# Kernel optimization log

Hardware: AMD Instinct MI355X
Metric: run time of the kernel (lower is better)

## Reference

```python
import jax, jax.numpy as jnp
import numpy as np

B, P, N = 1024, 100, 101
EMB, H, DK = 128, 8, 16
SQRT_EMB = 11.313708498984761
CLIP = 10.0


def setup_inputs() -> dict:
    key = jax.random.key(0)
    ks = jax.random.split(key, 12)
    inp = {
        "encoded_last_node": jax.random.normal(ks[0], (B, P, EMB), jnp.float32),
        "load": jax.random.uniform(ks[1], (B, P), jnp.float32),
        "time": jax.random.uniform(ks[2], (B, P), jnp.float32),
        "length": jax.random.uniform(ks[3], (B, P), jnp.float32),
        "route_open": jax.random.uniform(ks[4], (B, P), jnp.float32),
        "ninf_mask": jnp.zeros((B, P, N), jnp.float32),
        "encoded_nodes": jax.random.normal(ks[5], (B, N, EMB), jnp.float32),
        # weights stored [in, out]
        "Wq": jax.random.normal(ks[6], (EMB + 4, H * DK), jnp.float32) * 0.05,
        "Wk": jax.random.normal(ks[7], (EMB, H * DK), jnp.float32) * 0.05,
        "Wv": jax.random.normal(ks[8], (EMB, H * DK), jnp.float32) * 0.05,
        "Wc": jax.random.normal(ks[9], (H * DK, EMB), jnp.float32) * 0.05,
        "bc": jax.random.normal(ks[10], (EMB,), jnp.float32) * 0.05,
    }
    return inp


def _heads(x):
    # [B, n, H*DK] -> [B, H, n, DK]
    b, n, _ = x.shape
    return x.reshape(b, n, H, DK).transpose(0, 2, 1, 3)


def reference(encoded_last_node, load, time, length, route_open, ninf_mask,
              encoded_nodes, Wq, Wk, Wv, Wc, bc):
    # set_kv
    k = _heads(encoded_nodes @ Wk)            # [B,H,N,DK]
    v = _heads(encoded_nodes @ Wv)            # [B,H,N,DK]
    # forward
    input_cat = jnp.concatenate(
        [encoded_last_node, load[:, :, None], time[:, :, None],
         length[:, :, None], route_open[:, :, None]], axis=2)  # [B,P,EMB+4]
    q = _heads(input_cat @ Wq)                # [B,H,P,DK]
    score = jnp.einsum('bhpd,bhnd->bhpn', q, k) / jnp.sqrt(jnp.float32(DK))
    score = score + ninf_mask[:, None, :, :]
    weights = jax.nn.softmax(score, axis=3)
    out = jnp.einsum('bhpn,bhnd->bhpd', weights, v)
    out_concat = out.transpose(0, 2, 1, 3).reshape(out.shape[0], out.shape[2], H * DK)
    mh = out_concat @ Wc + bc                 # [B,P,EMB]
    score2 = jnp.einsum('bpe,bne->bpn', mh, encoded_nodes) / SQRT_EMB
    score2 = CLIP * jnp.tanh(score2) + ninf_mask
    probs = jax.nn.softmax(score2, axis=2)
    return probs
```

## Files before the change

### kernel.cpp

```cpp
#include <hip/hip_runtime.h>
#include <stdint.h>

#define B_    1024
#define P_    100
#define N_    101
#define EMB_  128
#define H_    8
#define DK_   16

#define ROWS  112
#define KSTR  136

typedef uint16_t bf16;
typedef __attribute__((ext_vector_type(8))) short short8;
typedef __attribute__((ext_vector_type(4))) float float4v;

struct F4 { float x, y, z, w; };

#define L2E 1.4426950408889634f

#if __has_builtin(__builtin_amdgcn_exp2f)
#define EXP2(x) __builtin_amdgcn_exp2f(x)
#else
#define EXP2(x) exp2f(x)
#endif
#if __has_builtin(__builtin_amdgcn_rcpf)
#define RCP(x) __builtin_amdgcn_rcpf(x)
#else
#define RCP(x) (1.0f / (x))
#endif

__device__ __forceinline__ float b2f(bf16 u) {
    union { uint32_t i; float f; } c; c.i = ((uint32_t)u) << 16; return c.f;
}
__device__ __forceinline__ bf16 f2b(float f) {
    union { float f; uint32_t i; } c; c.f = f;
    return (bf16)((c.i + 0x8000u) >> 16);
}
__device__ __forceinline__ uint32_t pk2(float a, float b) {
    union { float f; uint32_t i; } ca, cb; ca.f = a; cb.f = b;
    return __builtin_amdgcn_perm(cb.i + 0x8000u, ca.i + 0x8000u, 0x07060302u);
}

__device__ __forceinline__ void stage_m(const float* __restrict__ src, int nrows,
                                        bf16* __restrict__ dst, int tid) {
    for (int i = tid; i < ROWS * 32; i += 1024) {
        int r = i >> 5, c = (i & 31) << 2;
        uint32_t p0 = 0, p1 = 0;
        if (r < nrows) {
            float4 v = *(const float4*)(src + (size_t)r * EMB_ + c);
            p0 = pk2(v.x, v.y); p1 = pk2(v.z, v.w);
        }
        uint32_t* d = (uint32_t*)(dst + r * KSTR + c);
        d[0] = p0; d[1] = p1;
    }
}

__global__ __launch_bounds__(256)
void prep_wT(const float* __restrict__ Wq, const float* __restrict__ Wk,
             const float* __restrict__ Wv, const float* __restrict__ Wc,
             bf16* __restrict__ ws) {
    int idx = blockIdx.x * 256 + threadIdx.x;
    int w = idx >> 14, rem = idx & 16383;
    int k = rem >> 7, o = rem & 127;
    const float* W = (w == 0) ? Wk : (w == 1) ? Wv : (w == 2) ? Wq : Wc;
    ws[((size_t)w << 14) + o * 128 + k] = f2b(W[(size_t)k * 128 + o]);
}

__global__ __launch_bounds__(1024, 4)
void vrp_kernel(const float* __restrict__ eln,
                const float* __restrict__ load_,
                const float* __restrict__ time_,
                const float* __restrict__ len_,
                const float* __restrict__ open_,
                const float* __restrict__ mask_,
                const float* __restrict__ enc_,
                const float* __restrict__ Wq,
                const float* __restrict__ bc,
                const bf16* __restrict__ wsWT,
                float* __restrict__ out)
{
    const int b    = blockIdx.x;
    const int tid  = threadIdx.x;
    const int wave = tid >> 6;
    const int lane = tid & 63;
    const int lr = lane & 15, lq = lane >> 4, lk = lq << 3;

    __shared__ bf16 smem[78336];
    __shared__ float sS4[ROWS * 4];
    __shared__ float sWq4[4 * EMB_];
    bf16* const R1 = smem;
    bf16* const R2 = smem + 15232;
    bf16* const R3 = smem + 30464;
    bf16* const R4 = smem + 47872;
    bf16* const R5 = smem + 63104;

    const bf16* WkT = wsWT;
    const bf16* WvT = wsWT + 16384;
    const bf16* WqT = wsWT + 32768;
    const bf16* WcT = wsWT + 49152;

    const float* encB  = enc_  + (size_t)b * N_ * EMB_;
    const float* elnB  = eln   + (size_t)b * P_ * EMB_;
    const float* maskB = mask_ + (size_t)b * P_ * N_;
    float*       outB  = out   + (size_t)b * P_ * N_;

    stage_m(encB, N_, R1, tid);
    stage_m(elnB, P_, R5, tid);
    if (tid < 512) {
        int d = tid >> 2, c = 112 + ((tid & 3) << 2);
        uint32_t* z = (uint32_t*)(R3 + d * KSTR + c);
        z[0] = 0; z[1] = 0;
    }
    if (tid < ROWS * 4) {
        int r = tid >> 2, j = tid & 3;
        float v = 0.f;
        if (r < P_) {
            const float* s4 = (j == 0) ? load_ : (j == 1) ? time_
                             : (j == 2) ? len_ : open_;
            v = s4[(size_t)b * P_ + r];
        }
        sS4[r * 4 + j] = v;
    }
    if (tid < 512) {
        int j = tid >> 7, c = tid & 127;
        sWq4[j * EMB_ + c] = Wq[(size_t)(EMB_ + j) * EMB_ + c];
    }
    __syncthreads();

    {
        const int col = 16 * (wave & 7) + lr;
        const int mt0 = (wave >> 3) ? 4 : 0;
        const int mt1 = (wave >> 3) ? 7 : 4;
        short8 bk[4], bv[4], bq[4];
        {
            const bf16* rk = WkT + (size_t)col * 128 + lk;
            const bf16* rv = WvT + (size_t)col * 128 + lk;
            const bf16* rq = WqT + (size_t)col * 128 + lk;
            #pragma unroll
            for (int s = 0; s < 4; ++s) {
                bk[s] = *(const short8*)(rk + s * 32);
                bv[s] = *(const short8*)(rv + s * 32);
                bq[s] = *(const short8*)(rq + s * 32);
            }
        }
        float w0 = sWq4[col], w1 = sWq4[EMB_ + col];
        float w2 = sWq4[2 * EMB_ + col], w3 = sWq4[3 * EMB_ + col];
        for (int mt = mt0; mt < mt1; ++mt) {
            short8 a[4];
            #pragma unroll
            for (int s = 0; s < 4; ++s)
                a[s] = *(const short8*)(R1 + (mt * 16 + lr) * KSTR + s * 32 + lk);
            float4v ck = {0.f, 0.f, 0.f, 0.f}, cv = {0.f, 0.f, 0.f, 0.f};
            #pragma unroll
            for (int s = 0; s < 4; ++s) {
                ck = __builtin_amdgcn_mfma_f32_16x16x32_bf16(a[s], bk[s], ck, 0, 0, 0);
                cv = __builtin_amdgcn_mfma_f32_16x16x32_bf16(a[s], bv[s], cv, 0, 0, 0);
            }
            int n0 = mt * 16 + (lq << 2);
            #pragma unroll
            for (int r = 0; r < 4; ++r)
                R2[(n0 + r) * KSTR + col] = f2b(ck[r]);
            uint32_t* d = (uint32_t*)(R3 + col * KSTR + n0);
            d[0] = pk2(cv[0], cv[1]);
            d[1] = pk2(cv[2], cv[3]);
            short8 aq[4];
            #pragma unroll
            for (int s = 0; s < 4; ++s)
                aq[s] = *(const short8*)(R5 + (mt * 16 + lr) * KSTR + s * 32 + lk);
            float4v cq = {0.f, 0.f, 0.f, 0.f};
            #pragma unroll
            for (int s = 0; s < 4; ++s)
                cq = __builtin_amdgcn_mfma_f32_16x16x32_bf16(aq[s], bq[s], cq, 0, 0, 0);
            int row0 = mt * 16 + (lq << 2);
            #pragma unroll
            for (int r = 0; r < 4; ++r) {
                const float* s4 = sS4 + (row0 + r) * 4;
                float acc = cq[r] + s4[0] * w0 + s4[1] * w1 + s4[2] * w2 + s4[3] * w3;
                R4[(row0 + r) * KSTR + col] = f2b(acc * (0.25f * L2E));
            }
        }
    }
    __syncthreads();

    const int hg = (wave >= 7) ? 1 : 0;
    const int pt = wave - hg * 7;
    float msk2[7][4];
    float4v o4[4];
    short8 q0, q1;
    if (wave < 14) {
        {
            const int p = pt * 16 + lr;
            const bool pvalid = (p < P_);
            const float* mrow = maskB + (size_t)(pvalid ? p : 0) * N_;
            #pragma unroll
            for (int nt = 0; nt < 6; ++nt) {
                int nb = nt * 16 + (lq << 2);
                F4 mv = *(const F4*)(mrow + nb);
                msk2[nt][0] = pvalid ? mv.x * L2E : 0.f;
                msk2[nt][1] = pvalid ? mv.y * L2E : 0.f;
                msk2[nt][2] = pvalid ? mv.z * L2E : 0.f;
                msk2[nt][3] = pvalid ? mv.w * L2E : 0.f;
            }
            if (lq == 0) {
                F4 mv = *(const F4*)(mrow + 96);
                msk2[6][0] = pvalid ? mv.x * L2E : 0.f;
                msk2[6][1] = pvalid ? mv.y * L2E : 0.f;
                msk2[6][2] = pvalid ? mv.z * L2E : 0.f;
                msk2[6][3] = pvalid ? mv.w * L2E : 0.f;
            } else if (lq == 1) {
                msk2[6][0] = pvalid ? mrow[100] * L2E : 0.f;
                msk2[6][1] = -3.0e38f; msk2[6][2] = -3.0e38f; msk2[6][3] = -3.0e38f;
            } else {
                msk2[6][0] = -3.0e38f; msk2[6][1] = -3.0e38f;
                msk2[6][2] = -3.0e38f; msk2[6][3] = -3.0e38f;
            }
        }
        q0 = *(const short8*)(R4 + (pt * 16 + lr) * KSTR + hg * 64 + lk);
        q1 = *(const short8*)(R4 + (pt * 16 + lr) * KSTR + hg * 64 + 32 + lk);
    }
    __syncthreads();
    if (wave < 14) {
        bf16* Pbuf = hg ? R4 : R5;
        {
            uint32_t* z = (uint32_t*)(Pbuf + (pt * 16 + lr) * KSTR + 112 + (lq << 2));
            z[0] = 0; z[1] = 0;
        }
        #pragma unroll
        for (int hh = 0; hh < 4; ++hh) {
            int h  = hg * 4 + hh;
            int k0 = hg * 64 + (hh >> 1) * 32;
            short8 bq = (hh < 2) ? q0 : q1;
            if ((lq >> 1) != (hh & 1)) bq = (short8){0,0,0,0,0,0,0,0};
            float sc[7][4];
            #pragma unroll
            for (int nt = 0; nt < 7; ++nt) {
                short8 ak = *(const short8*)(R2 + (nt * 16 + lr) * KSTR + k0 + lk);
                float4v cc = {msk2[nt][0], msk2[nt][1], msk2[nt][2], msk2[nt][3]};
                cc = __builtin_amdgcn_mfma_f32_16x16x32_bf16(ak, bq, cc, 0, 0, 0);
                #pragma unroll
                for (int r = 0; r < 4; ++r) sc[nt][r] = cc[r];
            }
            float mm[7];
            #pragma unroll
            for (int nt = 0; nt < 7; ++nt)
                mm[nt] = fmaxf(fmaxf(sc[nt][0], sc[nt][1]),
                               fmaxf(sc[nt][2], sc[nt][3]));
            float m = fmaxf(fmaxf(fmaxf(mm[0], mm[1]), fmaxf(mm[2], mm[3])),
                            fmaxf(fmaxf(mm[4], mm[5]), mm[6]));
            m = fmaxf(m, __shfl_xor(m, 16));
            m = fmaxf(m, __shfl_xor(m, 32));
            float s0 = 0.f, s1 = 0.f, s2 = 0.f, s3 = 0.f;
            #pragma unroll
            for (int nt = 0; nt < 7; ++nt) {
                float e0 = EXP2(sc[nt][0] - m); sc[nt][0] = e0; s0 += e0;
                float e1 = EXP2(sc[nt][1] - m); sc[nt][1] = e1; s1 += e1;
                float e2 = EXP2(sc[nt][2] - m); sc[nt][2] = e2; s2 += e2;
                float e3 = EXP2(sc[nt][3] - m); sc[nt][3] = e3; s3 += e3;
            }
            float su = (s0 + s1) + (s2 + s3);
            su += __shfl_xor(su, 16);
            su += __shfl_xor(su, 32);
            float inv = RCP(su);
            #pragma unroll
            for (int nt = 0; nt < 7; ++nt) {
                uint32_t* d = (uint32_t*)(Pbuf + (pt * 16 + lr) * KSTR
                                          + nt * 16 + (lq << 2));
                d[0] = pk2(sc[nt][0] * inv, sc[nt][1] * inv);
                d[1] = pk2(sc[nt][2] * inv, sc[nt][3] * inv);
            }
            float4v o = {0.f, 0.f, 0.f, 0.f};
            #pragma unroll
            for (int ks = 0; ks < 128; ks += 32) {
                short8 a2 = *(const short8*)(Pbuf + (pt * 16 + lr) * KSTR + ks + lk);
                short8 b2 = *(const short8*)(R3 + (h * 16 + lr) * KSTR + ks + lk);
                o = __builtin_amdgcn_mfma_f32_16x16x32_bf16(a2, b2, o, 0, 0, 0);
            }
            o4[hh] = o;
        }
    }
    __syncthreads();

    if (wave < 14) {
        #pragma unroll
        for (int hh = 0; hh < 4; ++hh) {
            int h = hg * 4 + hh;
            #pragma unroll
            for (int r = 0; r < 4; ++r)
                R4[(pt * 16 + (lq << 2) + r) * KSTR + h * 16 + lr] = f2b(o4[hh][r]);
        }
    }
    __syncthreads();

    {
        const int col = 16 * (wave & 7) + lr;
        const int mt0 = (wave >> 3) ? 4 : 0;
        const int mt1 = (wave >> 3) ? 7 : 4;
        short8 bw[4];
        {
            const bf16* rc = WcT + (size_t)col * 128 + lk;
            #pragma unroll
            for (int s = 0; s < 4; ++s) bw[s] = *(const short8*)(rc + s * 32);
        }
        float bcv = bc[col];
        for (int mt = mt0; mt < mt1; ++mt) {
            short8 a[4];
            #pragma unroll
            for (int s = 0; s < 4; ++s)
                a[s] = *(const short8*)(R4 + (mt * 16 + lr) * KSTR + s * 32 + lk);
            float4v c = {0.f, 0.f, 0.f, 0.f};
            #pragma unroll
            for (int s = 0; s < 4; ++s)
                c = __builtin_amdgcn_mfma_f32_16x16x32_bf16(a[s], bw[s], c, 0, 0, 0);
            int row0 = mt * 16 + (lq << 2);
            #pragma unroll
            for (int r = 0; r < 4; ++r) {
                float m = c[r] + bcv;
                bf16 hb = f2b(m);
                R5[(row0 + r) * KSTR + col] = hb;
                R2[(row0 + r) * KSTR + col] = f2b(m - b2f(hb));
            }
        }
    }
    __syncthreads();

    if (wave < 7) {
        const int pt2 = wave;
        short8 bhi[4], blo[4];
        #pragma unroll
        for (int s = 0; s < 4; ++s) {
            bhi[s] = *(const short8*)(R5 + (pt2 * 16 + lr) * KSTR + s * 32 + lk);
            blo[s] = *(const short8*)(R2 + (pt2 * 16 + lr) * KSTR + s * 32 + lk);
        }
        float sc[7][4];
        #pragma unroll
        for (int nt = 0; nt < 7; ++nt) {
            float4v cc = {0.f, 0.f, 0.f, 0.f};
            #pragma unroll
            for (int s = 0; s < 4; ++s) {
                short8 ae = *(const short8*)(R1 + (nt * 16 + lr) * KSTR + s * 32 + lk);
                cc = __builtin_amdgcn_mfma_f32_16x16x32_bf16(ae, bhi[s], cc, 0, 0, 0);
                cc = __builtin_amdgcn_mfma_f32_16x16x32_bf16(ae, blo[s], cc, 0, 0, 0);
            }
            #pragma unroll
            for (int r = 0; r < 4; ++r) {
                float y = EXP2(cc[r] * (0.08838834764831845f * 2.0f * L2E));
                float t = fmaf(-2.0f, RCP(y + 1.0f), 1.0f);
                sc[nt][r] = fmaf(10.0f * L2E, t, msk2[nt][r]);
            }
        }
        const float mF = 10.0f * L2E;
        float s0 = 0.f, s1 = 0.f, s2 = 0.f, s3 = 0.f;
        #pragma unroll
        for (int nt = 0; nt < 7; ++nt) {
            float e0 = EXP2(sc[nt][0] - mF); sc[nt][0] = e0; s0 += e0;
            float e1 = EXP2(sc[nt][1] - mF); sc[nt][1] = e1; s1 += e1;
            float e2 = EXP2(sc[nt][2] - mF); sc[nt][2] = e2; s2 += e2;
            float e3 = EXP2(sc[nt][3] - mF); sc[nt][3] = e3; s3 += e3;
        }
        float su = (s0 + s1) + (s2 + s3);
        su += __shfl_xor(su, 16);
        su += __shfl_xor(su, 32);
        float inv = RCP(su);
        const int p = pt2 * 16 + lr;
        if (p < P_) {
            float* orow = outB + (size_t)p * N_;
            #pragma unroll
            for (int nt = 0; nt < 6; ++nt) {
                F4 ov = { sc[nt][0] * inv, sc[nt][1] * inv,
                          sc[nt][2] * inv, sc[nt][3] * inv };
                *(F4*)(orow + nt * 16 + (lq << 2)) = ov;
            }
            if (lq == 0) {
                F4 ov = { sc[6][0] * inv, sc[6][1] * inv,
                          sc[6][2] * inv, sc[6][3] * inv };
                *(F4*)(orow + 96) = ov;
            } else if (lq == 1) {
                orow[100] = sc[6][0] * inv;
            }
        }
    }
}

extern "C" void kernel_launch(void* const* d_in, const int* in_sizes, int n_in,
                              void* d_out, int out_size, void* d_ws, size_t ws_size,
                              hipStream_t stream) {
    const float* eln   = (const float*)d_in[0];
    const float* load_ = (const float*)d_in[1];
    const float* time_ = (const float*)d_in[2];
    const float* len_  = (const float*)d_in[3];
    const float* open_ = (const float*)d_in[4];
    const float* mask_ = (const float*)d_in[5];
    const float* enc_  = (const float*)d_in[6];
    const float* Wq    = (const float*)d_in[7];
    const float* Wk    = (const float*)d_in[8];
    const float* Wv    = (const float*)d_in[9];
    const float* Wc    = (const float*)d_in[10];
    const float* bc    = (const float*)d_in[11];
    float* out = (float*)d_out;
    bf16* wsWT = (bf16*)d_ws;

    prep_wT<<<dim3(256), dim3(256), 0, stream>>>(Wq, Wk, Wv, Wc, wsWT);
    vrp_kernel<<<dim3(B_), dim3(1024), 0, stream>>>(
        eln, load_, time_, len_, open_, mask_, enc_, Wq, bc, wsWT, out);
}
```

Before: 271.4 us.

## Make blocks persistent over four batches and prefetch next batch into registers

The grid shrinks from one block per batch to 256 persistent blocks that each loop over four batch elements. The next batch's encoded_nodes, last-node embeddings and scalar features are loaded into registers mid-iteration, so their global latency can overlap the attention and output compute of the current batch. This also cuts block launch and setup overhead. In exchange, each block now holds extra registers for the prefetch buffers, and with only 256 blocks there may be too few waves in flight to hide latency on a GPU with many CUs.

```diff
diff --git a/kernel.cpp b/kernel.cpp
--- a/kernel.cpp
+++ b/kernel.cpp
@@ -7,6 +7,8 @@
 #define EMB_  128
 #define H_    8
 #define DK_   16
+#define GRID_ 256
+#define NPER_ (B_ / GRID_)
 
 #define ROWS  112
 #define KSTR  136
@@ -42,17 +44,50 @@
     return __builtin_amdgcn_perm(cb.i + 0x8000u, ca.i + 0x8000u, 0x07060302u);
 }
 
-__device__ __forceinline__ void stage_m(const float* __restrict__ src, int nrows,
-                                        bf16* __restrict__ dst, int tid) {
-    for (int i = tid; i < ROWS * 32; i += 1024) {
-        int r = i >> 5, c = (i & 31) << 2;
-        uint32_t p0 = 0, p1 = 0;
-        if (r < nrows) {
-            float4 v = *(const float4*)(src + (size_t)r * EMB_ + c);
-            p0 = pk2(v.x, v.y); p1 = pk2(v.z, v.w);
-        }
-        uint32_t* d = (uint32_t*)(dst + r * KSTR + c);
-        d[0] = p0; d[1] = p1;
+__device__ __forceinline__ void stage_load(const float* __restrict__ encB,
+                                           const float* __restrict__ elnB,
+                                           const float* __restrict__ load_,
+                                           const float* __restrict__ time_,
+                                           const float* __restrict__ len_,
+                                           const float* __restrict__ open_,
+                                           int b, int tid,
+                                           float4 (&e)[4], float4 (&c)[4],
+                                           float& s4v)
+{
+    #pragma unroll
+    for (int j = 0; j < 4; ++j) {
+        int i = tid + j * 1024;
+        float4 z = {0.f, 0.f, 0.f, 0.f};
+        e[j] = z; c[j] = z;
+        if (i < ROWS * 32) {
+            int r = i >> 5, cc = (i & 31) << 2;
+            if (r < N_) e[j] = *(const float4*)(encB + (size_t)r * EMB_ + cc);
+            if (r < P_) c[j] = *(const float4*)(elnB + (size_t)r * EMB_ + cc);
+        }
+    }
+    s4v = 0.f;
+    if (tid < ROWS * 4) {
+        int r = tid >> 2, jj = tid & 3;
+        if (r < P_) {
+            const float* s4 = (jj == 0) ? load_ : (jj == 1) ? time_
+                             : (jj == 2) ? len_ : open_;
+            s4v = s4[(size_t)b * P_ + r];
+        }
+    }
+}
+
+__device__ __forceinline__ void stage_write(const float4 (&v)[4],
+                                            bf16* __restrict__ dst, int tid)
+{
+    #pragma unroll
+    for (int j = 0; j < 4; ++j) {
+        int i = tid + j * 1024;
+        if (i < ROWS * 32) {
+            int r = i >> 5, cc = (i & 31) << 2;
+            uint32_t* d = (uint32_t*)(dst + r * KSTR + cc);
+            d[0] = pk2(v[j].x, v[j].y);
+            d[1] = pk2(v[j].z, v[j].w);
+        }
     }
 }
 
@@ -80,7 +115,6 @@
                 const bf16* __restrict__ wsWT,
                 float* __restrict__ out)
 {
-    const int b    = blockIdx.x;
     const int tid  = threadIdx.x;
     const int wave = tid >> 6;
     const int lane = tid & 63;
@@ -100,96 +134,38 @@
     const bf16* WqT = wsWT + 32768;
     const bf16* WcT = wsWT + 49152;
 
-    const float* encB  = enc_  + (size_t)b * N_ * EMB_;
-    const float* elnB  = eln   + (size_t)b * P_ * EMB_;
-    const float* maskB = mask_ + (size_t)b * P_ * N_;
-    float*       outB  = out   + (size_t)b * P_ * N_;
-
-    stage_m(encB, N_, R1, tid);
-    stage_m(elnB, P_, R5, tid);
     if (tid < 512) {
         int d = tid >> 2, c = 112 + ((tid & 3) << 2);
         uint32_t* z = (uint32_t*)(R3 + d * KSTR + c);
         z[0] = 0; z[1] = 0;
     }
-    if (tid < ROWS * 4) {
-        int r = tid >> 2, j = tid & 3;
-        float v = 0.f;
-        if (r < P_) {
-            const float* s4 = (j == 0) ? load_ : (j == 1) ? time_
-                             : (j == 2) ? len_ : open_;
-            v = s4[(size_t)b * P_ + r];
-        }
-        sS4[r * 4 + j] = v;
-    }
     if (tid < 512) {
         int j = tid >> 7, c = tid & 127;
         sWq4[j * EMB_ + c] = Wq[(size_t)(EMB_ + j) * EMB_ + c];
     }
-    __syncthreads();
-
+
+    float4 ereg[4], creg[4];
+    float s4v;
     {
-        const int col = 16 * (wave & 7) + lr;
-        const int mt0 = (wave >> 3) ? 4 : 0;
-        const int mt1 = (wave >> 3) ? 7 : 4;
-        short8 bk[4], bv[4], bq[4];
-        {
-            const bf16* rk = WkT + (size_t)col * 128 + lk;
-            const bf16* rv = WvT + (size_t)col * 128 + lk;
-            const bf16* rq = WqT + (size_t)col * 128 + lk;
-            #pragma unroll
-            for (int s = 0; s < 4; ++s) {
-                bk[s] = *(const short8*)(rk + s * 32);
-                bv[s] = *(const short8*)(rv + s * 32);
-                bq[s] = *(const short8*)(rq + s * 32);
-            }
-        }
-        float w0 = sWq4[col], w1 = sWq4[EMB_ + col];
-        float w2 = sWq4[2 * EMB_ + col], w3 = sWq4[3 * EMB_ + col];
-        for (int mt = mt0; mt < mt1; ++mt) {
-            short8 a[4];
-            #pragma unroll
-            for (int s = 0; s < 4; ++s)
-                a[s] = *(const short8*)(R1 + (mt * 16 + lr) * KSTR + s * 32 + lk);
-            float4v ck = {0.f, 0.f, 0.f, 0.f}, cv = {0.f, 0.f, 0.f, 0.f};
-            #pragma unroll
-            for (int s = 0; s < 4; ++s) {
-                ck = __builtin_amdgcn_mfma_f32_16x16x32_bf16(a[s], bk[s], ck, 0, 0, 0);
-                cv = __builtin_amdgcn_mfma_f32_16x16x32_bf16(a[s], bv[s], cv, 0, 0, 0);
-            }
-            int n0 = mt * 16 + (lq << 2);
-            #pragma unroll
-            for (int r = 0; r < 4; ++r)
-                R2[(n0 + r) * KSTR + col] = f2b(ck[r]);
-            uint32_t* d = (uint32_t*)(R3 + col * KSTR + n0);
-            d[0] = pk2(cv[0], cv[1]);
-            d[1] = pk2(cv[2], cv[3]);
-            short8 aq[4];
-            #pragma unroll
-            for (int s = 0; s < 4; ++s)
-                aq[s] = *(const short8*)(R5 + (mt * 16 + lr) * KSTR + s * 32 + lk);
-            float4v cq = {0.f, 0.f, 0.f, 0.f};
-            #pragma unroll
-            for (int s = 0; s < 4; ++s)
-                cq = __builtin_amdgcn_mfma_f32_16x16x32_bf16(aq[s], bq[s], cq, 0, 0, 0);
-            int row0 = mt * 16 + (lq << 2);
-            #pragma unroll
-            for (int r = 0; r < 4; ++r) {
-                const float* s4 = sS4 + (row0 + r) * 4;
-                float acc = cq[r] + s4[0] * w0 + s4[1] * w1 + s4[2] * w2 + s4[3] * w3;
-                R4[(row0 + r) * KSTR + col] = f2b(acc * (0.25f * L2E));
-            }
-        }
-    }
-    __syncthreads();
-
-    const int hg = (wave >= 7) ? 1 : 0;
-    const int pt = wave - hg * 7;
-    float msk2[7][4];
-    float4v o4[4];
-    short8 q0, q1;
-    if (wave < 14) {
-        {
+        const int b0 = blockIdx.x * NPER_;
+        stage_load(enc_ + (size_t)b0 * N_ * EMB_, eln + (size_t)b0 * P_ * EMB_,
+                   load_, time_, len_, open_, b0, tid, ereg, creg, s4v);
+    }
+
+    for (int s = 0; s < NPER_; ++s) {
+        const int b = blockIdx.x * NPER_ + s;
+        const float* maskB = mask_ + (size_t)b * P_ * N_;
+        float*       outB  = out   + (size_t)b * P_ * N_;
+
+        stage_write(ereg, R1, tid);
+        stage_write(creg, R5, tid);
+        if (tid < ROWS * 4) sS4[tid] = s4v;
+        __syncthreads();
+
+        const int hg = (wave >= 7) ? 1 : 0;
+        const int pt = wave - hg * 7;
+        float msk2[7][4];
+        if (wave < 14) {
             const int p = pt * 16 + lr;
             const bool pvalid = (p < P_);
             const float* mrow = maskB + (size_t)(pvalid ? p : 0) * N_;
@@ -216,169 +192,237 @@
                 msk2[6][2] = -3.0e38f; msk2[6][3] = -3.0e38f;
             }
         }
-        q0 = *(const short8*)(R4 + (pt * 16 + lr) * KSTR + hg * 64 + lk);
-        q1 = *(const short8*)(R4 + (pt * 16 + lr) * KSTR + hg * 64 + 32 + lk);
-    }
-    __syncthreads();
-    if (wave < 14) {
-        bf16* Pbuf = hg ? R4 : R5;
+
         {
-            uint32_t* z = (uint32_t*)(Pbuf + (pt * 16 + lr) * KSTR + 112 + (lq << 2));
-            z[0] = 0; z[1] = 0;
-        }
-        #pragma unroll
-        for (int hh = 0; hh < 4; ++hh) {
-            int h  = hg * 4 + hh;
-            int k0 = hg * 64 + (hh >> 1) * 32;
-            short8 bq = (hh < 2) ? q0 : q1;
-            if ((lq >> 1) != (hh & 1)) bq = (short8){0,0,0,0,0,0,0,0};
+            const int col = 16 * (wave & 7) + lr;
+            const int mt0 = (wave >> 3) ? 4 : 0;
+            const int mt1 = (wave >> 3) ? 7 : 4;
+            short8 bk[4], bv[4], bq[4];
+            {
+                const bf16* rk = WkT + (size_t)col * 128 + lk;
+                const bf16* rv = WvT + (size_t)col * 128 + lk;
+                const bf16* rq = WqT + (size_t)col * 128 + lk;
+                #pragma unroll
+                for (int ss = 0; ss < 4; ++ss) {
+                    bk[ss] = *(const short8*)(rk + ss * 32);
+                    bv[ss] = *(const short8*)(rv + ss * 32);
+                    bq[ss] = *(const short8*)(rq + ss * 32);
+                }
+            }
+            float w0 = sWq4[col], w1 = sWq4[EMB_ + col];
+            float w2 = sWq4[2 * EMB_ + col], w3 = sWq4[3 * EMB_ + col];
+            for (int mt = mt0; mt < mt1; ++mt) {
+                short8 a[4];
+                #pragma unroll
+                for (int ss = 0; ss < 4; ++ss)
+                    a[ss] = *(const short8*)(R1 + (mt * 16 + lr) * KSTR + ss * 32 + lk);
+                float4v ck = {0.f, 0.f, 0.f, 0.f}, cv = {0.f, 0.f, 0.f, 0.f};
+                #pragma unroll
+                for (int ss = 0; ss < 4; ++ss) {
+                    ck = __builtin_amdgcn_mfma_f32_16x16x32_bf16(a[ss], bk[ss], ck, 0, 0, 0);
+                    cv = __builtin_amdgcn_mfma_f32_16x16x32_bf16(a[ss], bv[ss], cv, 0, 0, 0);
+                }
+                int n0 = mt * 16 + (lq << 2);
+                #pragma unroll
+                for (int r = 0; r < 4; ++r)
+                    R2[(n0 + r) * KSTR + col] = f2b(ck[r]);
+                uint32_t* d = (uint32_t*)(R3 + col * KSTR + n0);
+                d[0] = pk2(cv[0], cv[1]);
+                d[1] = pk2(cv[2], cv[3]);
+                short8 aq[4];
+                #pragma unroll
+                for (int ss = 0; ss < 4; ++ss)
+                    aq[ss] = *(const short8*)(R5 + (mt * 16 + lr) * KSTR + ss * 32 + lk);
+                float4v cq = {0.f, 0.f, 0.f, 0.f};
+                #pragma unroll
+                for (int ss = 0; ss < 4; ++ss)
+                    cq = __builtin_amdgcn_mfma_f32_16x16x32_bf16(aq[ss], bq[ss], cq, 0, 0, 0);
+                int row0 = mt * 16 + (lq << 2);
+                #pragma unroll
+                for (int r = 0; r < 4; ++r) {
+                    const float* s4 = sS4 + (row0 + r) * 4;
+                    float acc = cq[r] + s4[0] * w0 + s4[1] * w1 + s4[2] * w2 + s4[3] * w3;
+                    R4[(row0 + r) * KSTR + col] = f2b(acc * (0.25f * L2E));
+                }
+            }
+        }
+        __syncthreads();
+
+        short8 q0, q1;
+        if (wave < 14) {
+            q0 = *(const short8*)(R4 + (pt * 16 + lr) * KSTR + hg * 64 + lk);
+            q1 = *(const short8*)(R4 + (pt * 16 + lr) * KSTR + hg * 64 + 32 + lk);
+        }
+        __syncthreads();
+
+        if (s + 1 < NPER_) {
+            const int bn = b + 1;
+            stage_load(enc_ + (size_t)bn * N_ * EMB_, eln + (size_t)bn * P_ * EMB_,
+                       load_, time_, len_, open_, bn, tid, ereg, creg, s4v);
+        }
+
+        float4v o4[4];
+        if (wave < 14) {
+            bf16* Pbuf = hg ? R4 : R5;
+            {
+                uint32_t* z = (uint32_t*)(Pbuf + (pt * 16 + lr) * KSTR + 112 + (lq << 2));
+                z[0] = 0; z[1] = 0;
+            }
+            #pragma unroll
+            for (int hh = 0; hh < 4; ++hh) {
+                int h  = hg * 4 + hh;
+                int k0 = hg * 64 + (hh >> 1) * 32;
+                short8 bq = (hh < 2) ? q0 : q1;
+                if ((lq >> 1) != (hh & 1)) bq = (short8){0,0,0,0,0,0,0,0};
+                float sc[7][4];
+                #pragma unroll
+                for (int nt = 0; nt < 7; ++nt) {
+                    short8 ak = *(const short8*)(R2 + (nt * 16 + lr) * KSTR + k0 + lk);
+                    float4v cc = {msk2[nt][0], msk2[nt][1], msk2[nt][2], msk2[nt][3]};
+                    cc = __builtin_amdgcn_mfma_f32_16x16x32_bf16(ak, bq, cc, 0, 0, 0);
+                    #pragma unroll
+                    for (int r = 0; r < 4; ++r) sc[nt][r] = cc[r];
+                }
+                float mm[7];
+                #pragma unroll
+                for (int nt = 0; nt < 7; ++nt)
+                    mm[nt] = fmaxf(fmaxf(sc[nt][0], sc[nt][1]),
+                                   fmaxf(sc[nt][2], sc[nt][3]));
+                float m = fmaxf(fmaxf(fmaxf(mm[0], mm[1]), fmaxf(mm[2], mm[3])),
+                                fmaxf(fmaxf(mm[4], mm[5]), mm[6]));
+                m = fmaxf(m, __shfl_xor(m, 16));
+                m = fmaxf(m, __shfl_xor(m, 32));
+                float s0 = 0.f, s1 = 0.f, s2 = 0.f, s3 = 0.f;
+                #pragma unroll
+                for (int nt = 0; nt < 7; ++nt) {
+                    float e0 = EXP2(sc[nt][0] - m); sc[nt][0] = e0; s0 += e0;
+                    float e1 = EXP2(sc[nt][1] - m); sc[nt][1] = e1; s1 += e1;
+                    float e2 = EXP2(sc[nt][2] - m); sc[nt][2] = e2; s2 += e2;
+                    float e3 = EXP2(sc[nt][3] - m); sc[nt][3] = e3; s3 += e3;
+                }
+                float su = (s0 + s1) + (s2 + s3);
+                su += __shfl_xor(su, 16);
+                su += __shfl_xor(su, 32);
+                float inv = RCP(su);
+                #pragma unroll
+                for (int nt = 0; nt < 7; ++nt) {
+                    uint32_t* d = (uint32_t*)(Pbuf + (pt * 16 + lr) * KSTR
+                                              + nt * 16 + (lq << 2));
+                    d[0] = pk2(sc[nt][0] * inv, sc[nt][1] * inv);
+                    d[1] = pk2(sc[nt][2] * inv, sc[nt][3] * inv);
+                }
+                float4v o = {0.f, 0.f, 0.f, 0.f};
+                #pragma unroll
+                for (int ks = 0; ks < 128; ks += 32) {
+                    short8 a2 = *(const short8*)(Pbuf + (pt * 16 + lr) * KSTR + ks + lk);
+                    short8 b2 = *(const short8*)(R3 + (h * 16 + lr) * KSTR + ks + lk);
+                    o = __builtin_amdgcn_mfma_f32_16x16x32_bf16(a2, b2, o, 0, 0, 0);
+                }
+                o4[hh] = o;
+            }
+        }
+        __syncthreads();
+
+        if (wave < 14) {
+            #pragma unroll
+            for (int hh = 0; hh < 4; ++hh) {
+                int h = hg * 4 + hh;
+                #pragma unroll
+                for (int r = 0; r < 4; ++r)
+                    R4[(pt * 16 + (lq << 2) + r) * KSTR + h * 16 + lr] = f2b(o4[hh][r]);
+            }
+        }
+        __syncthreads();
+
+        {
+            const int col = 16 * (wave & 7) + lr;
+            const int mt0 = (wave >> 3) ? 4 : 0;
+            const int mt1 = (wave >> 3) ? 7 : 4;
+            short8 bw[4];
+            {
+                const bf16* rc = WcT + (size_t)col * 128 + lk;
+                #pragma unroll
+                for (int ss = 0; ss < 4; ++ss) bw[ss] = *(const short8*)(rc + ss * 32);
+            }
+            float bcv = bc[col];
+            for (int mt = mt0; mt < mt1; ++mt) {
+                short8 a[4];
+                #pragma unroll
+                for (int ss = 0; ss < 4; ++ss)
+                    a[ss] = *(const short8*)(R4 + (mt * 16 + lr) * KSTR + ss * 32 + lk);
+                float4v c = {0.f, 0.f, 0.f, 0.f};
+                #pragma unroll
+                for (int ss = 0; ss < 4; ++ss)
+                    c = __builtin_amdgcn_mfma_f32_16x16x32_bf16(a[ss], bw[ss], c, 0, 0, 0);
+                int row0 = mt * 16 + (lq << 2);
+                #pragma unroll
+                for (int r = 0; r < 4; ++r) {
+                    float m = c[r] + bcv;
+                    bf16 hb = f2b(m);
+                    R5[(row0 + r) * KSTR + col] = hb;
+                    R2[(row0 + r) * KSTR + col] = f2b(m - b2f(hb));
+                }
+            }
+        }
+        __syncthreads();
+
+        if (wave < 7) {
+            const int pt2 = wave;
+            short8 bhi[4], blo[4];
+            #pragma unroll
+            for (int ss = 0; ss < 4; ++ss) {
+                bhi[ss] = *(const short8*)(R5 + (pt2 * 16 + lr) * KSTR + ss * 32 + lk);
+                blo[ss] = *(const short8*)(R2 + (pt2 * 16 + lr) * KSTR + ss * 32 + lk);
+            }
             float sc[7][4];
             #pragma unroll
             for (int nt = 0; nt < 7; ++nt) {
-                short8 ak = *(const short8*)(R2 + (nt * 16 + lr) * KSTR + k0 + lk);
-                float4v cc = {msk2[nt][0], msk2[nt][1], msk2[nt][2], msk2[nt][3]};
-                cc = __builtin_amdgcn_mfma_f32_16x16x32_bf16(ak, bq, cc, 0, 0, 0);
-                #pragma unroll
-                for (int r = 0; r < 4; ++r) sc[nt][r] = cc[r];
-            }
-            float mm[7];
-            #pragma unroll
-            for (int nt = 0; nt < 7; ++nt)
-                mm[nt] = fmaxf(fmaxf(sc[nt][0], sc[nt][1]),
-                               fmaxf(sc[nt][2], sc[nt][3]));
-            float m = fmaxf(fmaxf(fmaxf(mm[0], mm[1]), fmaxf(mm[2], mm[3])),
-                            fmaxf(fmaxf(mm[4], mm[5]), mm[6]));
-            m = fmaxf(m, __shfl_xor(m, 16));
-            m = fmaxf(m, __shfl_xor(m, 32));
+                float4v cc = {0.f, 0.f, 0.f, 0.f};
+                #pragma unroll
+                for (int ss = 0; ss < 4; ++ss) {
+                    short8 ae = *(const short8*)(R1 + (nt * 16 + lr) * KSTR + ss * 32 + lk);
+                    cc = __builtin_amdgcn_mfma_f32_16x16x32_bf16(ae, bhi[ss], cc, 0, 0, 0);
+                    cc = __builtin_amdgcn_mfma_f32_16x16x32_bf16(ae, blo[ss], cc, 0, 0, 0);
+                }
+                #pragma unroll
+                for (int r = 0; r < 4; ++r) {
+                    float y = EXP2(cc[r] * (0.08838834764831845f * 2.0f * L2E));
+                    float t = fmaf(-2.0f, RCP(y + 1.0f), 1.0f);
+                    sc[nt][r] = fmaf(10.0f * L2E, t, msk2[nt][r]);
+                }
+            }
+            const float mF = 10.0f * L2E;
             float s0 = 0.f, s1 = 0.f, s2 = 0.f, s3 = 0.f;
             #pragma unroll
             for (int nt = 0; nt < 7; ++nt) {
-                float e0 = EXP2(sc[nt][0] - m); sc[nt][0] = e0; s0 += e0;
-                float e1 = EXP2(sc[nt][1] - m); sc[nt][1] = e1; s1 += e1;
-                float e2 = EXP2(sc[nt][2] - m); sc[nt][2] = e2; s2 += e2;
-                float e3 = EXP2(sc[nt][3] - m); sc[nt][3] = e3; s3 += e3;
+                float e0 = EXP2(sc[nt][0] - mF); sc[nt][0] = e0; s0 += e0;
+                float e1 = EXP2(sc[nt][1] - mF); sc[nt][1] = e1; s1 += e1;
+                float e2 = EXP2(sc[nt][2] - mF); sc[nt][2] = e2; s2 += e2;
+                float e3 = EXP2(sc[nt][3] - mF); sc[nt][3] = e3; s3 += e3;
             }
             float su = (s0 + s1) + (s2 + s3);
             su += __shfl_xor(su, 16);
             su += __shfl_xor(su, 32);
             float inv = RCP(su);
-            #pragma unroll
-            for (int nt = 0; nt < 7; ++nt) {
-                uint32_t* d = (uint32_t*)(Pbuf + (pt * 16 + lr) * KSTR
-                                          + nt * 16 + (lq << 2));
-                d[0] = pk2(sc[nt][0] * inv, sc[nt][1] * inv);
-                d[1] = pk2(sc[nt][2] * inv, sc[nt][3] * inv);
-            }
-            float4v o = {0.f, 0.f, 0.f, 0.f};
-            #pragma unroll
-            for (int ks = 0; ks < 128; ks += 32) {
-                short8 a2 = *(const short8*)(Pbuf + (pt * 16 + lr) * KSTR + ks + lk);
-                short8 b2 = *(const short8*)(R3 + (h * 16 + lr) * KSTR + ks + lk);
-                o = __builtin_amdgcn_mfma_f32_16x16x32_bf16(a2, b2, o, 0, 0, 0);
-            }
-            o4[hh] = o;
-        }
-    }
-    __syncthreads();
-
-    if (wave < 14) {
-        #pragma unroll
-        for (int hh = 0; hh < 4; ++hh) {
-            int h = hg * 4 + hh;
-            #pragma unroll
-            for (int r = 0; r < 4; ++r)
-                R4[(pt * 16 + (lq << 2) + r) * KSTR + h * 16 + lr] = f2b(o4[hh][r]);
-        }
-    }
-    __syncthreads();
-
-    {
-        const int col = 16 * (wave & 7) + lr;
-        const int mt0 = (wave >> 3) ? 4 : 0;
-        const int mt1 = (wave >> 3) ? 7 : 4;
-        short8 bw[4];
-        {
-            const bf16* rc = WcT + (size_t)col * 128 + lk;
-            #pragma unroll
-            for (int s = 0; s < 4; ++s) bw[s] = *(const short8*)(rc + s * 32);
-        }
-        float bcv = bc[col];
-        for (int mt = mt0; mt < mt1; ++mt) {
-            short8 a[4];
-            #pragma unroll
-            for (int s = 0; s < 4; ++s)
-                a[s] = *(const short8*)(R4 + (mt * 16 + lr) * KSTR + s * 32 + lk);
-            float4v c = {0.f, 0.f, 0.f, 0.f};
-            #pragma unroll
-            for (int s = 0; s < 4; ++s)
-                c = __builtin_amdgcn_mfma_f32_16x16x32_bf16(a[s], bw[s], c, 0, 0, 0);
-            int row0 = mt * 16 + (lq << 2);
-            #pragma unroll
-            for (int r = 0; r < 4; ++r) {
-                float m = c[r] + bcv;
-                bf16 hb = f2b(m);
-                R5[(row0 + r) * KSTR + col] = hb;
-                R2[(row0 + r) * KSTR + col] = f2b(m - b2f(hb));
-            }
-        }
-    }
-    __syncthreads();
-
-    if (wave < 7) {
-        const int pt2 = wave;
-        short8 bhi[4], blo[4];
-        #pragma unroll
-        for (int s = 0; s < 4; ++s) {
-            bhi[s] = *(const short8*)(R5 + (pt2 * 16 + lr) * KSTR + s * 32 + lk);
-            blo[s] = *(const short8*)(R2 + (pt2 * 16 + lr) * KSTR + s * 32 + lk);
-        }
-        float sc[7][4];
-        #pragma unroll
-        for (int nt = 0; nt < 7; ++nt) {
-            float4v cc = {0.f, 0.f, 0.f, 0.f};
-            #pragma unroll
-            for (int s = 0; s < 4; ++s) {
-                short8 ae = *(const short8*)(R1 + (nt * 16 + lr) * KSTR + s * 32 + lk);
-                cc = __builtin_amdgcn_mfma_f32_16x16x32_bf16(ae, bhi[s], cc, 0, 0, 0);
-                cc = __builtin_amdgcn_mfma_f32_16x16x32_bf16(ae, blo[s], cc, 0, 0, 0);
-            }
-            #pragma unroll
-            for (int r = 0; r < 4; ++r) {
-                float y = EXP2(cc[r] * (0.08838834764831845f * 2.0f * L2E));
-                float t = fmaf(-2.0f, RCP(y + 1.0f), 1.0f);
-                sc[nt][r] = fmaf(10.0f * L2E, t, msk2[nt][r]);
-            }
-        }
-        const float mF = 10.0f * L2E;
-        float s0 = 0.f, s1 = 0.f, s2 = 0.f, s3 = 0.f;
-        #pragma unroll
-        for (int nt = 0; nt < 7; ++nt) {
-            float e0 = EXP2(sc[nt][0] - mF); sc[nt][0] = e0; s0 += e0;
-            float e1 = EXP2(sc[nt][1] - mF); sc[nt][1] = e1; s1 += e1;
-            float e2 = EXP2(sc[nt][2] - mF); sc[nt][2] = e2; s2 += e2;
-            float e3 = EXP2(sc[nt][3] - mF); sc[nt][3] = e3; s3 += e3;
-        }
-        float su = (s0 + s1) + (s2 + s3);
-        su += __shfl_xor(su, 16);
-        su += __shfl_xor(su, 32);
-        float inv = RCP(su);
-        const int p = pt2 * 16 + lr;
-        if (p < P_) {
-            float* orow = outB + (size_t)p * N_;
-            #pragma unroll
-            for (int nt = 0; nt < 6; ++nt) {
-                F4 ov = { sc[nt][0] * inv, sc[nt][1] * inv,
-                          sc[nt][2] * inv, sc[nt][3] * inv };
-                *(F4*)(orow + nt * 16 + (lq << 2)) = ov;
-            }
-            if (lq == 0) {
-                F4 ov = { sc[6][0] * inv, sc[6][1] * inv,
-                          sc[6][2] * inv, sc[6][3] * inv };
-                *(F4*)(orow + 96) = ov;
-            } else if (lq == 1) {
-                orow[100] = sc[6][0] * inv;
-            }
-        }
+            const int p = pt2 * 16 + lr;
+            if (p < P_) {
+                float* orow = outB + (size_t)p * N_;
+                #pragma unroll
+                for (int nt = 0; nt < 6; ++nt) {
+                    F4 ov = { sc[nt][0] * inv, sc[nt][1] * inv,
+                              sc[nt][2] * inv, sc[nt][3] * inv };
+                    *(F4*)(orow + nt * 16 + (lq << 2)) = ov;
+                }
+                if (lq == 0) {
+                    F4 ov = { sc[6][0] * inv, sc[6][1] * inv,
+                              sc[6][2] * inv, sc[6][3] * inv };
+                    *(F4*)(orow + 96) = ov;
+                } else if (lq == 1) {
+                    orow[100] = sc[6][0] * inv;
+                }
+            }
+        }
+        if (s + 1 < NPER_) __syncthreads();
     }
 }
 
@@ -401,6 +445,6 @@
     bf16* wsWT = (bf16*)d_ws;
 
     prep_wT<<<dim3(256), dim3(256), 0, stream>>>(Wq, Wk, Wv, Wc, wsWT);
-    vrp_kernel<<<dim3(B_), dim3(1024), 0, stream>>>(
+    vrp_kernel<<<dim3(GRID_), dim3(1024), 0, stream>>>(
         eln, load_, time_, len_, open_, mask_, enc_, Wq, bc, wsWT, out);
 }
```

After: 397.3 us. +46.4%, slower.
